# Kernel optimization log

Hardware: AMD Instinct MI355X
Metric: run time of the kernel (lower is better)

Reference implementation:

```python
import jax, jax.numpy as jnp
import numpy as np

BETA = 0.1  # sliced_fgw_distance default (forward does not override it)
EPS = 1e-12  # F.normalize eps


def setup_inputs() -> dict:
    key = jax.random.key(0)
    k1, k2, k3 = jax.random.split(key, 3)
    N, D, P = 2048, 512, 10
    z = jax.random.normal(k1, (N, D), dtype=jnp.float32)
    gmm_noise = jax.random.normal(k2, (N, D), dtype=jnp.float32)
    projections = jax.random.normal(k3, (D, P), dtype=jnp.float32)
    return {"z": z, "gmm_noise": gmm_noise, "projections": projections}


def _pairwise_sq_diff(a):
    # a: [N, P] -> [N, N, P] of (a_i - a_j)^2  (p=2, so abs()**2 == square)
    return (a[:, None, :] - a[None, :, :]) ** 2


def reference(z, gmm_noise, projections):
    # gmm_samples = F.normalize(randn_like(z)) : L2-normalize rows
    norm = jnp.maximum(jnp.linalg.norm(gmm_noise, axis=1, keepdims=True), EPS)
    gmm_samples = gmm_noise / norm  # [N, D]

    post = jnp.sort(z @ projections, axis=0)            # [N, P] ascending
    prior_proj = gmm_samples @ projections              # [N, P]
    prior1 = jnp.sort(prior_proj, axis=0)               # ascending
    prior2 = prior1[::-1]                               # descending sort

    post_diff = _pairwise_sq_diff(post)                 # [N, N, P]
    gw1 = jnp.mean((post_diff - _pairwise_sq_diff(prior1)) ** 2, axis=(0, 1))  # [P]
    gw2 = jnp.mean((post_diff - _pairwise_sq_diff(prior2)) ** 2, axis=(0, 1))  # [P]

    w1 = jnp.sum((post - prior1) ** 2, axis=0)          # [P]
    w2 = jnp.sum((post - prior2) ** 2, axis=0)          # [P]

    fgw1 = (1.0 - BETA) * w1 + BETA * gw1
    fgw2 = (1.0 - BETA) * w2 + BETA * gw2
    return jnp.mean(jnp.minimum(fgw1, fgw2))
```

## Files before the change

### kernel.cpp

```cpp
#include <hip/hip_runtime.h>
#include <math.h>

#define N_ROWS 2048
#define D_DIM 512
#define P_DIM 10

__device__ inline float wave_reduce_f(float v) {
#pragma unroll
  for (int off = 32; off > 0; off >>= 1) v += __shfl_down(v, off, 64);
  return v;
}

__device__ inline double wave_reduce_d(double v) {
#pragma unroll
  for (int off = 32; off > 0; off >>= 1) v += __shfl_down(v, off, 64);
  return v;
}

__device__ inline void wave_lds_fence() {
  asm volatile("" ::: "memory");
  __builtin_amdgcn_wave_barrier();
  asm volatile("" ::: "memory");
}

__global__ __launch_bounds__(256) void rc_proj_kernel(
    const float4* __restrict__ z4, const float4* __restrict__ g4,
    const float* __restrict__ proj, float* __restrict__ post_cm,
    float* __restrict__ prior_cm, float* __restrict__ out) {
  __shared__ float pl[P_DIM * D_DIM];
  for (int i = threadIdx.x; i < P_DIM * D_DIM; i += 256) {
    int e = i / P_DIM, p = i - e * P_DIM;
    pl[p * D_DIM + (e & 3) * 128 + (e >> 2)] = proj[i];
  }
  if (blockIdx.x == 0 && threadIdx.x == 0) out[0] = 0.f;
  __syncthreads();
  const int wave = threadIdx.x >> 6, lane = threadIdx.x & 63;
  const int row = blockIdx.x * 4 + wave;
  const float4* zr = z4 + (size_t)row * (D_DIM / 4);
  const float4* gr = g4 + (size_t)row * (D_DIM / 4);
  float4 zv[2], gv[2];
  zv[0] = zr[lane];
  zv[1] = zr[64 + lane];
  gv[0] = gr[lane];
  gv[1] = gr[64 + lane];
  float n2 = gv[0].x * gv[0].x + gv[0].y * gv[0].y + gv[0].z * gv[0].z +
             gv[0].w * gv[0].w + gv[1].x * gv[1].x + gv[1].y * gv[1].y +
             gv[1].z * gv[1].z + gv[1].w * gv[1].w;
  float az[P_DIM], ag[P_DIM];
#pragma unroll
  for (int p = 0; p < P_DIM; ++p) { az[p] = 0.f; ag[p] = 0.f; }
#pragma unroll
  for (int m = 0; m < 2; ++m) {
    const float zc[4] = {zv[m].x, zv[m].y, zv[m].z, zv[m].w};
    const float gc[4] = {gv[m].x, gv[m].y, gv[m].z, gv[m].w};
#pragma unroll
    for (int c = 0; c < 4; ++c) {
#pragma unroll
      for (int p = 0; p < P_DIM; ++p) {
        float w = pl[p * D_DIM + c * 128 + m * 64 + lane];
        az[p] += zc[c] * w;
        ag[p] += gc[c] * w;
      }
    }
  }
#pragma unroll
  for (int p = 0; p < P_DIM; ++p) {
    az[p] = wave_reduce_f(az[p]);
    ag[p] = wave_reduce_f(ag[p]);
  }
  n2 = wave_reduce_f(n2);
  if (lane == 0) {
    float inv = 1.f / fmaxf(sqrtf(n2), 1e-12f);
#pragma unroll
    for (int p = 0; p < P_DIM; ++p) {
      post_cm[p * N_ROWS + row] = az[p];
      prior_cm[p * N_ROWS + row] = ag[p] * inv;
    }
  }
}

__device__ inline double fgw_eval(double Sa, double Sb, double Sa2, double Sb2,
                                  double Sa3, double Sb3, double Sa4,
                                  double Sb4, double U1, double U2, double U3,
                                  double U4) {
  const double n = (double)N_ROWS;
  double T0 = Sa4 - 2.0 * U4 + Sb4;
  double T1 = Sa2 - Sb2;
  double T2 = Sa3 - U3;
  double T4 = U2 - Sb3;
  double gw = (2.0 * n * T0 + 2.0 * T1 * T1 - 8.0 * (T2 * Sa - T4 * Sb) +
               4.0 * (Sa2 * Sa2 - 2.0 * U1 * U1 + Sb2 * Sb2)) /
              (n * n);
  double w = Sa2 + Sb2 - 2.0 * U1;
  return 0.9 * w + 0.1 * gw;
}

__global__ __launch_bounds__(1024) void rc_sortstats_kernel(
    const float* __restrict__ post_cm, const float* __restrict__ prior_cm,
    float* __restrict__ out) {
  __shared__ float sa[N_ROWS];
  __shared__ float sb[N_ROWS];
  __shared__ double sm[16][16];
  const int p = blockIdx.x;
  const int tid = threadIdx.x;
  sa[tid] = post_cm[p * N_ROWS + tid];
  sa[tid + 1024] = post_cm[p * N_ROWS + tid + 1024];
  sb[tid] = prior_cm[p * N_ROWS + tid];
  sb[tid + 1024] = prior_cm[p * N_ROWS + tid + 1024];
  __syncthreads();
  bool prev_big = false;
  for (unsigned k = 2; k <= N_ROWS; k <<= 1) {
    for (unsigned j = k >> 1; j > 0; j >>= 1) {
      const bool big = (j >= 64);
      if (big || prev_big)
        __syncthreads();
      else
        wave_lds_fence();
      unsigned idx = ((tid & ~(j - 1)) << 1) | (tid & (j - 1));
      unsigned ixj = idx | j;
      const bool up = (idx & k) == 0;
      float x = sa[idx], y = sa[ixj];
      if (up ? (x > y) : (x < y)) { sa[idx] = y; sa[ixj] = x; }
      float u = sb[idx], v = sb[ixj];
      if (up ? (u > v) : (u < v)) { sb[idx] = v; sb[ixj] = u; }
      prev_big = big;
    }
  }
  __syncthreads();
  double S[16];
#pragma unroll
  for (int t = 0; t < 16; ++t) S[t] = 0.0;
  for (int i = tid; i < N_ROWS; i += 1024) {
    double a = (double)sa[i];
    double b = (double)sb[i];
    double br = (double)sb[N_ROWS - 1 - i];
    double a2 = a * a, b2 = b * b, br2 = br * br;
    S[0] += a;
    S[1] += b;
    S[2] += a2;
    S[3] += b2;
    S[4] += a2 * a;
    S[5] += b2 * b;
    S[6] += a2 * a2;
    S[7] += b2 * b2;
    S[8] += a * b;
    S[9] += a2 * b;
    S[10] += a * b2;
    S[11] += a2 * b2;
    S[12] += a * br;
    S[13] += a2 * br;
    S[14] += a * br2;
    S[15] += a2 * br2;
  }
#pragma unroll
  for (int t = 0; t < 16; ++t) S[t] = wave_reduce_d(S[t]);
  const int wave = tid >> 6, lane = tid & 63;
  if (lane == 0) {
#pragma unroll
    for (int t = 0; t < 16; ++t) sm[wave][t] = S[t];
  }
  __syncthreads();
  if (tid == 0) {
    double T[16];
#pragma unroll
    for (int t = 0; t < 16; ++t) {
      double acc = 0.0;
      for (int w = 0; w < 16; ++w) acc += sm[w][t];
      T[t] = acc;
    }
    double f1 = fgw_eval(T[0], T[1], T[2], T[3], T[4], T[5], T[6], T[7], T[8],
                         T[9], T[10], T[11]);
    double f2 = fgw_eval(T[0], T[1], T[2], T[3], T[4], T[5], T[6], T[7], T[12],
                         T[13], T[14], T[15]);
    atomicAdd(out, (float)(fmin(f1, f2) * (1.0 / P_DIM)));
  }
}

extern "C" void kernel_launch(void* const* d_in, const int* in_sizes, int n_in,
                              void* d_out, int out_size, void* d_ws,
                              size_t ws_size, hipStream_t stream) {
  const float4* z4 = (const float4*)d_in[0];
  const float4* g4 = (const float4*)d_in[1];
  const float* proj = (const float*)d_in[2];
  float* out = (float*)d_out;
  float* post_cm = (float*)d_ws;
  float* prior_cm = post_cm + N_ROWS * P_DIM;

  rc_proj_kernel<<<N_ROWS / 4, 256, 0, stream>>>(z4, g4, proj, post_cm,
                                                 prior_cm, out);
  rc_sortstats_kernel<<<P_DIM, 1024, 0, stream>>>(post_cm, prior_cm, out);
}
```

Before: 102.7 us.

## Replace per-column bitonic sort with parallel rank-counting sort across many blocks

Swaps the single-block-per-column bitonic sort, which runs on only 10 blocks with many barriers, for a counting-rank sort. Each element is packed into a unique 64-bit key (order-preserving float bits plus row index), and 160 blocks each compute the rank of one element per thread by comparing against all 2048 keys in its column, then scatter it to its sorted position. A separate stats kernel then computes the moment sums. This spreads the sort over far more CUs at the cost of O(N^2) comparisons per column, a 64-bit key write, and an extra kernel launch.

```diff
diff --git a/kernel.cpp b/kernel.cpp
--- a/kernel.cpp
+++ b/kernel.cpp
@@ -17,16 +17,16 @@
   return v;
 }
 
-__device__ inline void wave_lds_fence() {
-  asm volatile("" ::: "memory");
-  __builtin_amdgcn_wave_barrier();
-  asm volatile("" ::: "memory");
+__device__ inline unsigned long long sort_key(float v, int idx) {
+  unsigned u = __float_as_uint(v);
+  unsigned s = (u & 0x80000000u) ? ~u : (u | 0x80000000u);
+  return ((unsigned long long)s << 32) | (unsigned)idx;
 }
 
 __global__ __launch_bounds__(256) void rc_proj_kernel(
     const float4* __restrict__ z4, const float4* __restrict__ g4,
-    const float* __restrict__ proj, float* __restrict__ post_cm,
-    float* __restrict__ prior_cm, float* __restrict__ out) {
+    const float* __restrict__ proj, unsigned long long* __restrict__ keys,
+    float* __restrict__ out) {
   __shared__ float pl[P_DIM * D_DIM];
   for (int i = threadIdx.x; i < P_DIM * D_DIM; i += 256) {
     int e = i / P_DIM, p = i - e * P_DIM;
@@ -73,10 +73,24 @@
     float inv = 1.f / fmaxf(sqrtf(n2), 1e-12f);
 #pragma unroll
     for (int p = 0; p < P_DIM; ++p) {
-      post_cm[p * N_ROWS + row] = az[p];
-      prior_cm[p * N_ROWS + row] = ag[p] * inv;
+      keys[p * N_ROWS + row] = sort_key(az[p], row);
+      keys[(P_DIM + p) * N_ROWS + row] = sort_key(ag[p] * inv, row);
     }
   }
+}
+
+__global__ __launch_bounds__(256) void rc_rank_kernel(
+    const unsigned long long* __restrict__ keys, float* __restrict__ sorted) {
+  const int col = blockIdx.x >> 3;
+  const int i = ((blockIdx.x & 7) << 8) | threadIdx.x;
+  const unsigned long long* __restrict__ K = keys + col * N_ROWS;
+  const unsigned long long my = K[i];
+  int r = 0;
+#pragma unroll 16
+  for (int j = 0; j < N_ROWS; ++j) r += (K[j] < my) ? 1 : 0;
+  unsigned s = (unsigned)(my >> 32);
+  unsigned u = (s & 0x80000000u) ? (s & 0x7FFFFFFFu) : ~s;
+  sorted[col * N_ROWS + r] = __uint_as_float(u);
 }
 
 __device__ inline double fgw_eval(double Sa, double Sb, double Sa2, double Sb2,
@@ -95,79 +109,50 @@
   return 0.9 * w + 0.1 * gw;
 }
 
-__global__ __launch_bounds__(1024) void rc_sortstats_kernel(
-    const float* __restrict__ post_cm, const float* __restrict__ prior_cm,
-    float* __restrict__ out) {
-  __shared__ float sa[N_ROWS];
-  __shared__ float sb[N_ROWS];
-  __shared__ double sm[16][16];
+__global__ __launch_bounds__(256) void rc_stats_kernel(
+    const float* __restrict__ sorted, float* __restrict__ out) {
   const int p = blockIdx.x;
-  const int tid = threadIdx.x;
-  sa[tid] = post_cm[p * N_ROWS + tid];
-  sa[tid + 1024] = post_cm[p * N_ROWS + tid + 1024];
-  sb[tid] = prior_cm[p * N_ROWS + tid];
-  sb[tid + 1024] = prior_cm[p * N_ROWS + tid + 1024];
-  __syncthreads();
-  bool prev_big = false;
-  for (unsigned k = 2; k <= N_ROWS; k <<= 1) {
-    for (unsigned j = k >> 1; j > 0; j >>= 1) {
-      const bool big = (j >= 64);
-      if (big || prev_big)
-        __syncthreads();
-      else
-        wave_lds_fence();
-      unsigned idx = ((tid & ~(j - 1)) << 1) | (tid & (j - 1));
-      unsigned ixj = idx | j;
-      const bool up = (idx & k) == 0;
-      float x = sa[idx], y = sa[ixj];
-      if (up ? (x > y) : (x < y)) { sa[idx] = y; sa[ixj] = x; }
-      float u = sb[idx], v = sb[ixj];
-      if (up ? (u > v) : (u < v)) { sb[idx] = v; sb[ixj] = u; }
-      prev_big = big;
-    }
-  }
-  __syncthreads();
+  const float* a = sorted + p * N_ROWS;
+  const float* b = sorted + (P_DIM + p) * N_ROWS;
   double S[16];
 #pragma unroll
   for (int t = 0; t < 16; ++t) S[t] = 0.0;
-  for (int i = tid; i < N_ROWS; i += 1024) {
-    double a = (double)sa[i];
-    double b = (double)sb[i];
-    double br = (double)sb[N_ROWS - 1 - i];
-    double a2 = a * a, b2 = b * b, br2 = br * br;
-    S[0] += a;
-    S[1] += b;
+  for (int i = threadIdx.x; i < N_ROWS; i += 256) {
+    double av = (double)a[i];
+    double bv = (double)b[i];
+    double br = (double)b[N_ROWS - 1 - i];
+    double a2 = av * av, b2 = bv * bv, br2 = br * br;
+    S[0] += av;
+    S[1] += bv;
     S[2] += a2;
     S[3] += b2;
-    S[4] += a2 * a;
-    S[5] += b2 * b;
+    S[4] += a2 * av;
+    S[5] += b2 * bv;
     S[6] += a2 * a2;
     S[7] += b2 * b2;
-    S[8] += a * b;
-    S[9] += a2 * b;
-    S[10] += a * b2;
+    S[8] += av * bv;
+    S[9] += a2 * bv;
+    S[10] += av * b2;
     S[11] += a2 * b2;
-    S[12] += a * br;
+    S[12] += av * br;
     S[13] += a2 * br;
-    S[14] += a * br2;
+    S[14] += av * br2;
     S[15] += a2 * br2;
   }
 #pragma unroll
   for (int t = 0; t < 16; ++t) S[t] = wave_reduce_d(S[t]);
-  const int wave = tid >> 6, lane = tid & 63;
+  __shared__ double sm[4][16];
+  const int wave = threadIdx.x >> 6, lane = threadIdx.x & 63;
   if (lane == 0) {
 #pragma unroll
     for (int t = 0; t < 16; ++t) sm[wave][t] = S[t];
   }
   __syncthreads();
-  if (tid == 0) {
+  if (threadIdx.x == 0) {
     double T[16];
 #pragma unroll
-    for (int t = 0; t < 16; ++t) {
-      double acc = 0.0;
-      for (int w = 0; w < 16; ++w) acc += sm[w][t];
-      T[t] = acc;
-    }
+    for (int t = 0; t < 16; ++t)
+      T[t] = sm[0][t] + sm[1][t] + sm[2][t] + sm[3][t];
     double f1 = fgw_eval(T[0], T[1], T[2], T[3], T[4], T[5], T[6], T[7], T[8],
                          T[9], T[10], T[11]);
     double f2 = fgw_eval(T[0], T[1], T[2], T[3], T[4], T[5], T[6], T[7], T[12],
@@ -183,10 +168,10 @@
   const float4* g4 = (const float4*)d_in[1];
   const float* proj = (const float*)d_in[2];
   float* out = (float*)d_out;
-  float* post_cm = (float*)d_ws;
-  float* prior_cm = post_cm + N_ROWS * P_DIM;
+  unsigned long long* keys = (unsigned long long*)d_ws;
+  float* sorted = (float*)(keys + 2 * P_DIM * N_ROWS);
 
-  rc_proj_kernel<<<N_ROWS / 4, 256, 0, stream>>>(z4, g4, proj, post_cm,
-                                                 prior_cm, out);
-  rc_sortstats_kernel<<<P_DIM, 1024, 0, stream>>>(post_cm, prior_cm, out);
+  rc_proj_kernel<<<N_ROWS / 4, 256, 0, stream>>>(z4, g4, proj, keys, out);
+  rc_rank_kernel<<<2 * P_DIM * 8, 256, 0, stream>>>(keys, sorted);
+  rc_stats_kernel<<<P_DIM, 256, 0, stream>>>(sorted, out);
 }
```

Measured after the change: 117.8 us. +14.7%, slower.
